# Kernel tuning notes

Hardware: AMD Instinct MI355X
Metric: run time of the kernel (lower is better)

The kernel has to match this reference:

```python
import jax, jax.numpy as jnp
import numpy as np

NUM_HEADS = 16


def setup_inputs() -> dict:
    key = jax.random.key(0)
    ks = jax.random.split(key, 9)
    B, S, D = 2, 2048, 1024
    scale = 1.0 / np.sqrt(D)
    return {
        "hidden_states": jax.random.normal(ks[0], (B, S, D), dtype=jnp.float32),
        "Wq": jax.random.normal(ks[1], (D, D), dtype=jnp.float32) * scale,
        "bq": jnp.zeros((D,), dtype=jnp.float32),
        "Wk": jax.random.normal(ks[2], (D, D), dtype=jnp.float32) * scale,
        "bk": jnp.zeros((D,), dtype=jnp.float32),
        "Wv": jax.random.normal(ks[3], (D, D), dtype=jnp.float32) * scale,
        "bv": jnp.zeros((D,), dtype=jnp.float32),
        "Wo": jax.random.normal(ks[4], (D, D), dtype=jnp.float32) * scale,
        "bo": jnp.zeros((D,), dtype=jnp.float32),
    }


def reference(hidden_states, Wq, bq, Wk, bk, Wv, bv, Wo, bo):
    B, S, D = hidden_states.shape
    H = NUM_HEADS
    hd = D // H
    # q/k/v projections (torch Linear uses x @ W.T + b)
    q = hidden_states @ Wq.T + bq
    k = hidden_states @ Wk.T + bk
    v = hidden_states @ Wv.T + bv
    # split heads: b s (h d) -> b h s d
    q = q.reshape(B, S, H, hd)
    k = k.reshape(B, S, H, hd)
    v = v.reshape(B, S, H, hd)
    # scaled dot-product attention (non-causal, no mask)
    scale = 1.0 / jnp.sqrt(jnp.asarray(hd, dtype=q.dtype))
    scores = jnp.einsum("bqhd,bkhd->bhqk", q, k) * scale
    probs = jax.nn.softmax(scores, axis=-1)
    attn = jnp.einsum("bhqk,bkhd->bqhd", probs, v)
    # merge heads and output projection
    attn = attn.reshape(B, S, D)
    return attn @ Wo.T + bo
```

## Files before the change

kernel.cpp:

```cpp
#include <hip/hip_runtime.h>

typedef short bf16x8 __attribute__((ext_vector_type(8)));
typedef short bf16x4 __attribute__((ext_vector_type(4)));
typedef float f32x4 __attribute__((ext_vector_type(4)));
typedef float float4v __attribute__((ext_vector_type(4)));
typedef unsigned short u16x8 __attribute__((ext_vector_type(8)));
typedef unsigned short u16x4 __attribute__((ext_vector_type(4)));

#define GLL16(g, l_) __builtin_amdgcn_global_load_lds( \
    (const __attribute__((address_space(1))) unsigned int*)(g), \
    (__attribute__((address_space(3))) unsigned int*)(l_), 16, 0, 0)

__device__ __forceinline__ unsigned short f2bf(float x) {
  unsigned u = __float_as_uint(x);
  u += 0x7fff + ((u >> 16) & 1);
  return (unsigned short)(u >> 16);
}

__device__ __forceinline__ unsigned cvtpk_bf16(float a, float b) {
  unsigned r;
  asm("v_cvt_pk_bf16_f32 %0, %1, %2" : "=v"(r) : "v"(a), "v"(b));
  return r;
}

__global__ __launch_bounds__(256) void cast_all_kernel(
    const float* __restrict__ X, const float* __restrict__ Wq,
    const float* __restrict__ Wk, const float* __restrict__ Wv,
    const float* __restrict__ Wo,
    unsigned short* __restrict__ Xb, unsigned short* __restrict__ Wb) {
  int bx = blockIdx.x;
  const float* src; unsigned short* dst; int rel;
  if (bx < 2048) { src = X; dst = Xb; rel = bx; }
  else {
    int wi = (bx - 2048) >> 9; rel = (bx - 2048) & 511;
    src = (wi == 0) ? Wq : (wi == 1) ? Wk : (wi == 2) ? Wv : Wo;
    dst = Wb + ((size_t)wi << 20);
  }
  size_t o = (size_t)rel * 2048 + (size_t)threadIdx.x * 8;
  const float4v* s4 = (const float4v*)(src + o);
  float4v v0 = s4[0], v1 = s4[1];
  u16x8 r;
  r[0]=f2bf(v0[0]); r[1]=f2bf(v0[1]); r[2]=f2bf(v0[2]); r[3]=f2bf(v0[3]);
  r[4]=f2bf(v1[0]); r[5]=f2bf(v1[1]); r[6]=f2bf(v1[2]); r[7]=f2bf(v1[3]);
  *(u16x8*)(dst + o) = r;
}

__device__ __forceinline__ void gemm_core_128(
    const unsigned short* __restrict__ A, const unsigned short* __restrict__ Bt,
    int m0, int n0, int K,
    unsigned short* lA, unsigned short* lB, f32x4 acc[4][4]) {
  const int t = threadIdx.x;
  const int l = t & 63;
  const int wr = t >> 7, wc = (t >> 6) & 1;
  const int srow = t >> 3, scol = (t & 7) * 8;
  const int l15 = l & 15, lhi = l >> 4;
  for (int kt = 0; kt < K; kt += 64) {
#pragma unroll
    for (int p = 0; p < 4; ++p) {
      GLL16(A  + (size_t)(m0 + p * 32 + srow) * K + kt + scol, lA + (p * 32 + srow) * 64 + scol);
      GLL16(Bt + (size_t)(n0 + p * 32 + srow) * K + kt + scol, lB + (p * 32 + srow) * 64 + scol);
    }
    asm volatile("s_waitcnt vmcnt(0)" ::: "memory");
    __syncthreads();
#pragma unroll
    for (int ks = 0; ks < 2; ++ks) {
      bf16x8 af[4], bfr[4];
#pragma unroll
      for (int i = 0; i < 4; ++i) {
        af[i]  = *(const bf16x8*)(lA + (wr * 64 + i * 16 + l15) * 64 + ks * 32 + lhi * 8);
        bfr[i] = *(const bf16x8*)(lB + (wc * 64 + i * 16 + l15) * 64 + ks * 32 + lhi * 8);
      }
#pragma unroll
      for (int i = 0; i < 4; ++i)
#pragma unroll
        for (int j = 0; j < 4; ++j)
          acc[i][j] = __builtin_amdgcn_mfma_f32_16x16x32_bf16(af[i], bfr[j], acc[i][j], 0, 0, 0);
    }
    __syncthreads();
  }
}

__global__ __launch_bounds__(512, 1) void qkv_gemm256_kernel(
    const unsigned short* __restrict__ Xb, const unsigned short* __restrict__ Wb,
    const float* __restrict__ bq, const float* __restrict__ bk, const float* __restrict__ bv,
    unsigned short* __restrict__ Q, unsigned short* __restrict__ Kd,
    unsigned short* __restrict__ Vt, float qscale) {
  __shared__ __align__(16) unsigned short lds[2][2][256 * 64];
  const int bx0 = blockIdx.x;
  const int bx = (bx0 & 7) * 24 + (bx0 >> 3);
  const int mb = bx / 12, nb = bx % 12;
  const int t = threadIdx.x, l = t & 63;
  const int wm = (t >> 6) >> 2, wn = (t >> 6) & 3;
  const int l15 = l & 15, lhi = l >> 4, sw7 = l15 & 7;

  const unsigned short* Ag = Xb + (size_t)(mb * 256) * 1024;
  const unsigned short* Bg = Wb + (size_t)(nb * 256) * 1024;

  const int slc = (t & 7) ^ ((t >> 3) & 7);
#define STAGE256(kt_, ba_, bb_)                                                  \
  {                                                                              \
    _Pragma("unroll")                                                            \
    for (int i_ = 0; i_ < 4; ++i_) {                                             \
      const int srow = (t >> 3) + i_ * 64;                                       \
      GLL16(Ag + (size_t)srow * 1024 + (kt_) + slc * 8, (ba_) + (srow * 8 + (t & 7)) * 8); \
      GLL16(Bg + (size_t)srow * 1024 + (kt_) + slc * 8, (bb_) + (srow * 8 + (t & 7)) * 8); \
    }                                                                            \
  }
#define RD256(base_, rowbase_) \
  (*(const bf16x8*)((const char*)(base_) + ((rowbase_) + l15) * 128 + ((KS256 * 4 + lhi) ^ sw7) * 16))

  f32x4 acc[8][4];
#pragma unroll
  for (int mi = 0; mi < 8; ++mi)
#pragma unroll
    for (int ni = 0; ni < 4; ++ni)
#pragma unroll
      for (int r0 = 0; r0 < 4; ++r0) acc[mi][ni][r0] = 0.f;

  STAGE256(0, &lds[0][0][0], &lds[0][1][0]);
  asm volatile("s_waitcnt vmcnt(0)" ::: "memory");
  __builtin_amdgcn_s_barrier();

  int cur = 0;
  for (int kt = 0; kt < 1024; kt += 64) {
    const unsigned short* bA = &lds[cur][0][0];
    const unsigned short* bB = &lds[cur][1][0];
    if (kt + 64 < 1024) STAGE256(kt + 64, &lds[cur ^ 1][0][0], &lds[cur ^ 1][1][0]);

    bf16x8 af[4][2], b0[2][2], b1[2][2];
#pragma unroll
    for (int ks = 0; ks < 2; ++ks) {
      const int KS256 = ks;
#pragma unroll
      for (int mi = 0; mi < 4; ++mi) af[mi][ks] = RD256(bA, wm * 128 + mi * 16);
#pragma unroll
      for (int ni = 0; ni < 2; ++ni) b0[ni][ks] = RD256(bB, wn * 64 + ni * 16);
    }
    __builtin_amdgcn_s_setprio(1);
#pragma unroll
    for (int mi = 0; mi < 4; ++mi)
#pragma unroll
      for (int ni = 0; ni < 2; ++ni)
#pragma unroll
        for (int ks = 0; ks < 2; ++ks)
          acc[mi][ni] = __builtin_amdgcn_mfma_f32_16x16x32_bf16(af[mi][ks], b0[ni][ks], acc[mi][ni], 0, 0, 0);
    __builtin_amdgcn_s_setprio(0);
    __builtin_amdgcn_s_barrier();

#pragma unroll
    for (int ks = 0; ks < 2; ++ks) {
      const int KS256 = ks;
#pragma unroll
      for (int ni = 0; ni < 2; ++ni) b1[ni][ks] = RD256(bB, wn * 64 + (ni + 2) * 16);
    }
    __builtin_amdgcn_s_setprio(1);
#pragma unroll
    for (int mi = 0; mi < 4; ++mi)
#pragma unroll
      for (int ni = 0; ni < 2; ++ni)
#pragma unroll
        for (int ks = 0; ks < 2; ++ks)
          acc[mi][ni + 2] = __builtin_amdgcn_mfma_f32_16x16x32_bf16(af[mi][ks], b1[ni][ks], acc[mi][ni + 2], 0, 0, 0);
    __builtin_amdgcn_s_setprio(0);
    __builtin_amdgcn_s_barrier();

#pragma unroll
    for (int ks = 0; ks < 2; ++ks) {
      const int KS256 = ks;
#pragma unroll
      for (int mi = 0; mi < 4; ++mi) af[mi][ks] = RD256(bA, wm * 128 + (mi + 4) * 16);
    }
    __builtin_amdgcn_s_setprio(1);
#pragma unroll
    for (int mi = 0; mi < 4; ++mi)
#pragma unroll
      for (int ni = 0; ni < 2; ++ni)
#pragma unroll
        for (int ks = 0; ks < 2; ++ks)
          acc[mi + 4][ni] = __builtin_amdgcn_mfma_f32_16x16x32_bf16(af[mi][ks], b0[ni][ks], acc[mi + 4][ni], 0, 0, 0);
    __builtin_amdgcn_s_setprio(0);
    __builtin_amdgcn_s_barrier();

    __builtin_amdgcn_s_setprio(1);
#pragma unroll
    for (int mi = 0; mi < 4; ++mi)
#pragma unroll
      for (int ni = 0; ni < 2; ++ni)
#pragma unroll
        for (int ks = 0; ks < 2; ++ks)
          acc[mi + 4][ni + 2] = __builtin_amdgcn_mfma_f32_16x16x32_bf16(af[mi][ks], b1[ni][ks], acc[mi + 4][ni + 2], 0, 0, 0);
    __builtin_amdgcn_s_setprio(0);
    asm volatile("s_waitcnt vmcnt(0)" ::: "memory");
    __builtin_amdgcn_s_barrier();
    cur ^= 1;
  }
#undef STAGE256
#undef RD256

  const int kind = nb >> 2;
  const float* bias = (kind == 0) ? bq : (kind == 1) ? bk : bv;
#pragma unroll
  for (int mi = 0; mi < 8; ++mi)
#pragma unroll
    for (int ni = 0; ni < 4; ++ni) {
      int gm0 = mb * 256 + wm * 128 + mi * 16 + lhi * 4;
      int gn = nb * 256 + wn * 64 + ni * 16 + l15;
      int gnk = gn & 1023;
      float bb_ = bias[gnk];
      if (kind == 2) {
        int h = gnk >> 6, d = gnk & 63;
        int batch = gm0 >> 11, s = gm0 & 2047;
        u16x4 pk;
#pragma unroll
        for (int r0 = 0; r0 < 4; ++r0) pk[r0] = f2bf(acc[mi][ni][r0] + bb_);
        *(u16x4*)(Vt + ((size_t)(batch * 16 + h) * 64 + d) * 2048 + s) = pk;
      } else if (kind == 0) {
#pragma unroll
        for (int r0 = 0; r0 < 4; ++r0)
          Q[(size_t)(gm0 + r0) * 1024 + gnk] = f2bf((acc[mi][ni][r0] + bb_) * qscale);
      } else {
#pragma unroll
        for (int r0 = 0; r0 < 4; ++r0)
          Kd[(size_t)(gm0 + r0) * 1024 + gnk] = f2bf(acc[mi][ni][r0] + bb_);
      }
    }
}

__global__ __launch_bounds__(256, 3) void attn_kernel(
    const unsigned short* __restrict__ Q, const unsigned short* __restrict__ Kd,
    const unsigned short* __restrict__ Vt, unsigned short* __restrict__ Ao) {
  __shared__ __align__(16) unsigned short lKV[3][8192];
  const int bx0 = blockIdx.x;
  const int bx = (bx0 & 7) * 64 + (bx0 >> 3);
  const int bh = bx >> 4, qb = bx & 15;
  const int b = bh >> 4, h = bh & 15;
  const int t = threadIdx.x, l = t & 63;
  const int l15 = l & 15, lhi = l >> 4;
  const int q0 = b * 2048 + qb * 128 + (t >> 6) * 32;
  const unsigned short* Qp = Q + (size_t)q0 * 1024 + h * 64;
  const unsigned short* Kp = Kd + (size_t)b * 2048 * 1024 + h * 64;
  const unsigned short* Vp = Vt + (size_t)bh * 64 * 2048;

  bf16x8 qa[2][2];
#pragma unroll
  for (int rf = 0; rf < 2; ++rf)
#pragma unroll
    for (int ks = 0; ks < 2; ++ks)
      qa[rf][ks] = *(const bf16x8*)(Qp + (size_t)(rf * 16 + l15) * 1024 + ks * 32 + lhi * 8);

  f32x4 acc[2][4];
  float lsum[2];
#pragma unroll
  for (int rf = 0; rf < 2; ++rf) {
    lsum[rf] = 0.f;
#pragma unroll
    for (int j = 0; j < 4; ++j)
#pragma unroll
      for (int r0 = 0; r0 < 4; ++r0) acc[rf][j][r0] = 0.f;
  }

#define STAGE_KV(kb_, buf_)                                                   \
  {                                                                           \
    { int j = t;       int row = j >> 3, lch = (j & 7) ^ (row & 7);           \
      GLL16(Kp + (size_t)((kb_) + row) * 1024 + lch * 8, (buf_) + j * 8); }   \
    { int j = t + 256; int row = j >> 3, lch = (j & 7) ^ (row & 7);           \
      GLL16(Kp + (size_t)((kb_) + row) * 1024 + lch * 8, (buf_) + j * 8); }   \
    { int j = t;       int row = j >> 3, lch = (j & 7) ^ (row & 7);           \
      GLL16(Vp + (size_t)row * 2048 + (kb_) + lch * 8, (buf_) + 4096 + j * 8); } \
    { int j = t + 256; int row = j >> 3, lch = (j & 7) ^ (row & 7);           \
      GLL16(Vp + (size_t)row * 2048 + (kb_) + lch * 8, (buf_) + 4096 + j * 8); } \
  }

  unsigned short* L0 = &lKV[0][0];
  STAGE_KV(0, L0);
  STAGE_KV(64, L0 + 8192);

  for (int ti = 0; ti < 32; ++ti) {
    const unsigned short* bK = L0 + (ti % 3) * 8192;
    const unsigned short* bV = bK + 4096;
    if (ti < 30) {
      unsigned short* nbuf = L0 + ((ti + 2) % 3) * 8192;
      STAGE_KV((ti + 2) * 64, nbuf);
      asm volatile("s_waitcnt vmcnt(8)" ::: "memory");
    } else if (ti == 30) {
      asm volatile("s_waitcnt vmcnt(4)" ::: "memory");
    } else {
      asm volatile("s_waitcnt vmcnt(0)" ::: "memory");
    }
    __builtin_amdgcn_s_barrier();

    f32x4 st[2][4];
#pragma unroll
    for (int rf = 0; rf < 2; ++rf)
#pragma unroll
      for (int cf = 0; cf < 4; ++cf)
#pragma unroll
        for (int r0 = 0; r0 < 4; ++r0) st[rf][cf][r0] = 0.f;
    __builtin_amdgcn_s_setprio(1);
#pragma unroll
    for (int ks = 0; ks < 2; ++ks) {
      bf16x8 kfr[4];
#pragma unroll
      for (int cf = 0; cf < 4; ++cf)
        kfr[cf] = *(const bf16x8*)(bK + (cf * 16 + l15) * 64 + (((ks * 4 + lhi) ^ (l15 & 7)) << 3));
#pragma unroll
      for (int rf = 0; rf < 2; ++rf)
#pragma unroll
        for (int cf = 0; cf < 4; ++cf)
          st[rf][cf] = __builtin_amdgcn_mfma_f32_16x16x32_bf16(kfr[cf], qa[rf][ks], st[rf][cf], 0, 0, 0);
    }
    __builtin_amdgcn_s_setprio(0);

    unsigned pk[2][4][2];
#pragma unroll
    for (int rf = 0; rf < 2; ++rf)
#pragma unroll
      for (int cf = 0; cf < 4; ++cf) {
        float p0 = __builtin_amdgcn_exp2f(st[rf][cf][0]);
        float p1 = __builtin_amdgcn_exp2f(st[rf][cf][1]);
        float p2 = __builtin_amdgcn_exp2f(st[rf][cf][2]);
        float p3 = __builtin_amdgcn_exp2f(st[rf][cf][3]);
        lsum[rf] += (p0 + p1) + (p2 + p3);
        pk[rf][cf][0] = cvtpk_bf16(p0, p1);
        pk[rf][cf][1] = cvtpk_bf16(p2, p3);
      }

    __builtin_amdgcn_s_setprio(1);
#pragma unroll
    for (int ks = 0; ks < 2; ++ks) {
      bf16x8 pa[2];
#pragma unroll
      for (int rf = 0; rf < 2; ++rf) {
        union { unsigned u[4]; bf16x8 v; } pu;
        pu.u[0] = pk[rf][2 * ks][0];     pu.u[1] = pk[rf][2 * ks][1];
        pu.u[2] = pk[rf][2 * ks + 1][0]; pu.u[3] = pk[rf][2 * ks + 1][1];
        pa[rf] = pu.v;
      }
#pragma unroll
      for (int df = 0; df < 4; ++df) {
        const int row = df * 16 + l15;
        const char* vb = (const char*)bV + row * 128;
        const int sw = (row & 7) << 4;
        bf16x4 lo = *(const bf16x4*)(vb + ((ks * 64 + lhi * 8) ^ sw));
        bf16x4 hi = *(const bf16x4*)(vb + ((ks * 64 + 32 + lhi * 8) ^ sw));
        bf16x8 vf = {lo[0], lo[1], lo[2], lo[3], hi[0], hi[1], hi[2], hi[3]};
#pragma unroll
        for (int rf = 0; rf < 2; ++rf)
          acc[rf][df] = __builtin_amdgcn_mfma_f32_16x16x32_bf16(pa[rf], vf, acc[rf][df], 0, 0, 0);
      }
    }
    __builtin_amdgcn_s_setprio(0);

    __builtin_amdgcn_s_barrier();
  }
#undef STAGE_KV

#pragma unroll
  for (int rf = 0; rf < 2; ++rf) {
    lsum[rf] += __shfl_xor(lsum[rf], 16);
    lsum[rf] += __shfl_xor(lsum[rf], 32);
  }
  float rn[2][4];
#pragma unroll
  for (int rf = 0; rf < 2; ++rf)
#pragma unroll
    for (int r0 = 0; r0 < 4; ++r0)
      rn[rf][r0] = 1.0f / __shfl(lsum[rf], lhi * 4 + r0);
#pragma unroll
  for (int rf = 0; rf < 2; ++rf)
#pragma unroll
    for (int r0 = 0; r0 < 4; ++r0) {
      int grow = q0 + rf * 16 + lhi * 4 + r0;
#pragma unroll
      for (int df = 0; df < 4; ++df) {
        int gcol = h * 64 + df * 16 + l15;
        Ao[(size_t)grow * 1024 + gcol] = f2bf(acc[rf][df][r0] * rn[rf][r0]);
      }
    }
}

__global__ __launch_bounds__(256) void out_gemm_kernel(
    const unsigned short* __restrict__ Ab, const unsigned short* __restrict__ Wob,
    const float* __restrict__ bo, float* __restrict__ Out) {
  __shared__ __align__(16) unsigned short lA[128 * 64];
  __shared__ __align__(16) unsigned short lB[128 * 64];
  const int bx0 = blockIdx.x;
  const int bx = (bx0 & 7) * 32 + (bx0 >> 3);
  const int mb = bx >> 3, nb = bx & 7;
  f32x4 acc[4][4];
#pragma unroll
  for (int i = 0; i < 4; ++i)
#pragma unroll
    for (int j = 0; j < 4; ++j)
#pragma unroll
      for (int r0 = 0; r0 < 4; ++r0) acc[i][j][r0] = 0.f;
  gemm_core_128(Ab, Wob, mb * 128, nb * 128, 1024, lA, lB, acc);
  const int t = threadIdx.x, l = t & 63;
  const int wr = t >> 7, wc = (t >> 6) & 1;
  const int l15 = l & 15, lhi = l >> 4;
#pragma unroll
  for (int i = 0; i < 4; ++i)
#pragma unroll
    for (int j = 0; j < 4; ++j) {
      int gn = nb * 128 + wc * 64 + j * 16 + l15;
      float bb_ = bo[gn];
      int gm0 = mb * 128 + wr * 64 + i * 16 + lhi * 4;
#pragma unroll
      for (int r0 = 0; r0 < 4; ++r0)
        Out[(size_t)(gm0 + r0) * 1024 + gn] = acc[i][j][r0] + bb_;
    }
}

extern "C" void kernel_launch(void* const* d_in, const int* in_sizes, int n_in,
                              void* d_out, int out_size, void* d_ws, size_t ws_size,
                              hipStream_t stream) {
  const float* X  = (const float*)d_in[0];
  const float* Wq = (const float*)d_in[1];
  const float* bq = (const float*)d_in[2];
  const float* Wk = (const float*)d_in[3];
  const float* bk = (const float*)d_in[4];
  const float* Wv = (const float*)d_in[5];
  const float* bv = (const float*)d_in[6];
  const float* Wo = (const float*)d_in[7];
  const float* bo = (const float*)d_in[8];
  char* ws = (char*)d_ws;
  unsigned short* Xb = (unsigned short*)(ws);
  unsigned short* Wb = (unsigned short*)(ws + ((size_t)8  << 20));
  unsigned short* Qb = (unsigned short*)(ws + ((size_t)16 << 20));
  unsigned short* Kb = (unsigned short*)(ws + ((size_t)24 << 20));
  unsigned short* Vt = (unsigned short*)(ws + ((size_t)32 << 20));
  unsigned short* Ab = (unsigned short*)(ws + ((size_t)40 << 20));

  const float qscale = 1.4426950408889634f / 8.0f;

  cast_all_kernel<<<4096, 256, 0, stream>>>(X, Wq, Wk, Wv, Wo, Xb, Wb);
  qkv_gemm256_kernel<<<192, 512, 0, stream>>>(Xb, Wb, bq, bk, bv, Qb, Kb, Vt, qscale);
  attn_kernel<<<512, 256, 0, stream>>>(Qb, Kb, Vt, Ab);
  out_gemm_kernel<<<256, 256, 0, stream>>>(Ab, Wb + ((size_t)3 << 20), bo, (float*)d_out);
}
```

Before: 118.3 us.

## Permute V layout, single-barrier attention pipeline, and 512-thread swizzled output GEMM

The QKV GEMM now writes V^T with a permuted sequence order inside each 64-block, so the attention kernel can read each V fragment with one 16-byte swizzled LDS load instead of two 8-byte loads. The attention loop moves its wait and barrier ahead of issuing the next KV prefetch, which drops the trailing per-iteration barrier. The output projection GEMM is rewritten to use 512 threads with XOR-swizzled LDS staging, aiming to cut bank conflicts and give more waves per tile. The reordered barrier and prefetch have to keep the triple buffer race-free, and the permuted V layout has to match the order of the P fragments exactly.

```diff
diff --git a/kernel.cpp b/kernel.cpp
--- a/kernel.cpp
+++ b/kernel.cpp
@@ -1,7 +1,6 @@
 #include <hip/hip_runtime.h>
 
 typedef short bf16x8 __attribute__((ext_vector_type(8)));
-typedef short bf16x4 __attribute__((ext_vector_type(4)));
 typedef float f32x4 __attribute__((ext_vector_type(4)));
 typedef float float4v __attribute__((ext_vector_type(4)));
 typedef unsigned short u16x8 __attribute__((ext_vector_type(8)));
@@ -45,41 +44,6 @@
   *(u16x8*)(dst + o) = r;
 }
 
-__device__ __forceinline__ void gemm_core_128(
-    const unsigned short* __restrict__ A, const unsigned short* __restrict__ Bt,
-    int m0, int n0, int K,
-    unsigned short* lA, unsigned short* lB, f32x4 acc[4][4]) {
-  const int t = threadIdx.x;
-  const int l = t & 63;
-  const int wr = t >> 7, wc = (t >> 6) & 1;
-  const int srow = t >> 3, scol = (t & 7) * 8;
-  const int l15 = l & 15, lhi = l >> 4;
-  for (int kt = 0; kt < K; kt += 64) {
-#pragma unroll
-    for (int p = 0; p < 4; ++p) {
-      GLL16(A  + (size_t)(m0 + p * 32 + srow) * K + kt + scol, lA + (p * 32 + srow) * 64 + scol);
-      GLL16(Bt + (size_t)(n0 + p * 32 + srow) * K + kt + scol, lB + (p * 32 + srow) * 64 + scol);
-    }
-    asm volatile("s_waitcnt vmcnt(0)" ::: "memory");
-    __syncthreads();
-#pragma unroll
-    for (int ks = 0; ks < 2; ++ks) {
-      bf16x8 af[4], bfr[4];
-#pragma unroll
-      for (int i = 0; i < 4; ++i) {
-        af[i]  = *(const bf16x8*)(lA + (wr * 64 + i * 16 + l15) * 64 + ks * 32 + lhi * 8);
-        bfr[i] = *(const bf16x8*)(lB + (wc * 64 + i * 16 + l15) * 64 + ks * 32 + lhi * 8);
-      }
-#pragma unroll
-      for (int i = 0; i < 4; ++i)
-#pragma unroll
-        for (int j = 0; j < 4; ++j)
-          acc[i][j] = __builtin_amdgcn_mfma_f32_16x16x32_bf16(af[i], bfr[j], acc[i][j], 0, 0, 0);
-    }
-    __syncthreads();
-  }
-}
-
 __global__ __launch_bounds__(512, 1) void qkv_gemm256_kernel(
     const unsigned short* __restrict__ Xb, const unsigned short* __restrict__ Wb,
     const float* __restrict__ bq, const float* __restrict__ bk, const float* __restrict__ bv,
@@ -210,10 +174,13 @@
       if (kind == 2) {
         int h = gnk >> 6, d = gnk & 63;
         int batch = gm0 >> 11, s = gm0 & 2047;
+        int sl = s & 63;
+        int slp = (sl & 32) | ((sl & 12) << 1) | ((sl & 16) >> 2);
+        int sp = (s & ~63) | slp;
         u16x4 pk;
 #pragma unroll
         for (int r0 = 0; r0 < 4; ++r0) pk[r0] = f2bf(acc[mi][ni][r0] + bb_);
-        *(u16x4*)(Vt + ((size_t)(batch * 16 + h) * 64 + d) * 2048 + s) = pk;
+        *(u16x4*)(Vt + ((size_t)(batch * 16 + h) * 64 + d) * 2048 + sp) = pk;
       } else if (kind == 0) {
 #pragma unroll
         for (int r0 = 0; r0 < 4; ++r0)
@@ -278,16 +245,16 @@
   for (int ti = 0; ti < 32; ++ti) {
     const unsigned short* bK = L0 + (ti % 3) * 8192;
     const unsigned short* bV = bK + 4096;
+    if (ti < 31) {
+      asm volatile("s_waitcnt vmcnt(4)" ::: "memory");
+    } else {
+      asm volatile("s_waitcnt vmcnt(0)" ::: "memory");
+    }
+    __builtin_amdgcn_s_barrier();
     if (ti < 30) {
       unsigned short* nbuf = L0 + ((ti + 2) % 3) * 8192;
       STAGE_KV((ti + 2) * 64, nbuf);
-      asm volatile("s_waitcnt vmcnt(8)" ::: "memory");
-    } else if (ti == 30) {
-      asm volatile("s_waitcnt vmcnt(4)" ::: "memory");
-    } else {
-      asm volatile("s_waitcnt vmcnt(0)" ::: "memory");
-    }
-    __builtin_amdgcn_s_barrier();
+    }
 
     f32x4 st[2][4];
 #pragma unroll
@@ -338,20 +305,13 @@
       }
 #pragma unroll
       for (int df = 0; df < 4; ++df) {
-        const int row = df * 16 + l15;
-        const char* vb = (const char*)bV + row * 128;
-        const int sw = (row & 7) << 4;
-        bf16x4 lo = *(const bf16x4*)(vb + ((ks * 64 + lhi * 8) ^ sw));
-        bf16x4 hi = *(const bf16x4*)(vb + ((ks * 64 + 32 + lhi * 8) ^ sw));
-        bf16x8 vf = {lo[0], lo[1], lo[2], lo[3], hi[0], hi[1], hi[2], hi[3]};
+        bf16x8 vf = *(const bf16x8*)(bV + (df * 16 + l15) * 64 + (((ks * 4 + lhi) ^ (l15 & 7)) << 3));
 #pragma unroll
         for (int rf = 0; rf < 2; ++rf)
           acc[rf][df] = __builtin_amdgcn_mfma_f32_16x16x32_bf16(pa[rf], vf, acc[rf][df], 0, 0, 0);
       }
     }
     __builtin_amdgcn_s_setprio(0);
-
-    __builtin_amdgcn_s_barrier();
   }
 #undef STAGE_KV
 
@@ -379,7 +339,7 @@
     }
 }
 
-__global__ __launch_bounds__(256) void out_gemm_kernel(
+__global__ __launch_bounds__(512) void out_gemm_kernel(
     const unsigned short* __restrict__ Ab, const unsigned short* __restrict__ Wob,
     const float* __restrict__ bo, float* __restrict__ Out) {
   __shared__ __align__(16) unsigned short lA[128 * 64];
@@ -387,24 +347,56 @@
   const int bx0 = blockIdx.x;
   const int bx = (bx0 & 7) * 32 + (bx0 >> 3);
   const int mb = bx >> 3, nb = bx & 7;
-  f32x4 acc[4][4];
-#pragma unroll
-  for (int i = 0; i < 4; ++i)
+  const int t = threadIdx.x, l = t & 63, w = t >> 6;
+  const int wr = w >> 1, wc = w & 1;
+  const int l15 = l & 15, lhi = l >> 4, sw7 = l15 & 7;
+  const unsigned short* Ag = Ab + (size_t)(mb * 128) * 1024;
+  const unsigned short* Bg = Wob + (size_t)(nb * 128) * 1024;
+
+  f32x4 acc[2][4];
+#pragma unroll
+  for (int i = 0; i < 2; ++i)
 #pragma unroll
     for (int j = 0; j < 4; ++j)
 #pragma unroll
       for (int r0 = 0; r0 < 4; ++r0) acc[i][j][r0] = 0.f;
-  gemm_core_128(Ab, Wob, mb * 128, nb * 128, 1024, lA, lB, acc);
-  const int t = threadIdx.x, l = t & 63;
-  const int wr = t >> 7, wc = (t >> 6) & 1;
-  const int l15 = l & 15, lhi = l >> 4;
-#pragma unroll
-  for (int i = 0; i < 4; ++i)
+
+  for (int kt = 0; kt < 1024; kt += 64) {
+    {
+      int row = t >> 3, lch = (t & 7) ^ (row & 7);
+      GLL16(Ag + (size_t)row * 1024 + kt + lch * 8, lA + t * 8);
+      GLL16(Bg + (size_t)row * 1024 + kt + lch * 8, lB + t * 8);
+      int j2 = t + 512, row2 = j2 >> 3, lch2 = (j2 & 7) ^ (row2 & 7);
+      GLL16(Ag + (size_t)row2 * 1024 + kt + lch2 * 8, lA + j2 * 8);
+      GLL16(Bg + (size_t)row2 * 1024 + kt + lch2 * 8, lB + j2 * 8);
+    }
+    asm volatile("s_waitcnt vmcnt(0)" ::: "memory");
+    __syncthreads();
+#pragma unroll
+    for (int ks = 0; ks < 2; ++ks) {
+      bf16x8 af[2], bfr[4];
+#pragma unroll
+      for (int i = 0; i < 2; ++i)
+        af[i] = *(const bf16x8*)(lA + (wr * 32 + i * 16 + l15) * 64 + (((ks * 4 + lhi) ^ sw7) << 3));
+#pragma unroll
+      for (int j = 0; j < 4; ++j)
+        bfr[j] = *(const bf16x8*)(lB + (wc * 64 + j * 16 + l15) * 64 + (((ks * 4 + lhi) ^ sw7) << 3));
+#pragma unroll
+      for (int i = 0; i < 2; ++i)
+#pragma unroll
+        for (int j = 0; j < 4; ++j)
+          acc[i][j] = __builtin_amdgcn_mfma_f32_16x16x32_bf16(af[i], bfr[j], acc[i][j], 0, 0, 0);
+    }
+    __syncthreads();
+  }
+
+#pragma unroll
+  for (int i = 0; i < 2; ++i)
 #pragma unroll
     for (int j = 0; j < 4; ++j) {
       int gn = nb * 128 + wc * 64 + j * 16 + l15;
       float bb_ = bo[gn];
-      int gm0 = mb * 128 + wr * 64 + i * 16 + lhi * 4;
+      int gm0 = mb * 128 + wr * 32 + i * 16 + lhi * 4;
 #pragma unroll
       for (int r0 = 0; r0 < 4; ++r0)
         Out[(size_t)(gm0 + r0) * 1024 + gn] = acc[i][j][r0] + bb_;
@@ -436,5 +428,5 @@
   cast_all_kernel<<<4096, 256, 0, stream>>>(X, Wq, Wk, Wv, Wo, Xb, Wb);
   qkv_gemm256_kernel<<<192, 512, 0, stream>>>(Xb, Wb, bq, bk, bv, Qb, Kb, Vt, qscale);
   attn_kernel<<<512, 256, 0, stream>>>(Qb, Kb, Vt, Ab);
-  out_gemm_kernel<<<256, 256, 0, stream>>>(Ab, Wb + ((size_t)3 << 20), bo, (float*)d_out);
-}
+  out_gemm_kernel<<<256, 512, 0, stream>>>(Ab, Wb + ((size_t)3 << 20), bo, (float*)d_out);
+}
```

Result: faster. 105.8 us (-10.6%).
